# Optimization experiments

Hardware: AMD Instinct MI355X
Metric: run time of the kernel (lower is better)

Reference implementation:

```python
import jax, jax.numpy as jnp
import numpy as np

NUM_ITERATIONS = 3

def squash(t, axis=-1):
    sq = jnp.clip(jnp.sum(t * t, axis=axis, keepdims=True), 1e-8, 1e4)
    norm = jnp.sqrt(sq)
    scale = sq / (1.0 + sq)
    return scale * (t / (norm + 1e-8))

def setup_inputs() -> dict:
    key = jax.random.key(0)
    k1, k2 = jax.random.split(key)
    B, N_in, N_out, D_in, D_out = 128, 1152, 10, 8, 16
    u = jax.random.normal(k1, (B, N_in, D_in), dtype=jnp.float32)
    W = jax.random.normal(k2, (N_in, N_out, D_out, D_in), dtype=jnp.float32) * 0.005
    return {"u": u, "W": W}

def reference(u, W):
    # u: [B, N_in, D_in]; W: [N_in, N_out, D_out, D_in]
    # u_hat: [B, N_in, N_out, D_out]
    u_hat = jnp.einsum('iodk,bik->biod', W, u)
    u_hat = jnp.clip(u_hat, -10.0, 10.0)
    B, N_in, N_out, _ = u_hat.shape
    b = jnp.zeros((B, N_in, N_out), dtype=u_hat.dtype)
    v = None
    for it in range(NUM_ITERATIONS):
        c = jax.nn.softmax(b, axis=2)                      # [B, N_in, N_out]
        s = jnp.einsum('bio,biod->bod', c, u_hat)          # [B, N_out, D_out]
        v = squash(s, axis=-1)                             # [B, N_out, D_out]
        if it < NUM_ITERATIONS - 1:
            agreement = jnp.einsum('biod,bod->bio', u_hat, v)
            b = b + jnp.clip(agreement, -10.0, 10.0)
    return v
```

## Files before the change

kernel.cpp:

```cpp
#include <hip/hip_runtime.h>
#include <cstddef>

#define NB    128
#define NIN   1152
#define NOUT  10
#define DOUT  16
#define OD    160
#define NSEG  18
#define SEGI  64
#define PGRID (NB * NSEG)

typedef __attribute__((ext_vector_type(4))) unsigned int u32x4;

#if __has_builtin(__builtin_amdgcn_fdot2_f32_bf16)
#define HAS_DOT2 1
typedef __attribute__((ext_vector_type(2))) __bf16 bf16x2;
__device__ __forceinline__ float dot2bf(unsigned w, unsigned uu, float c) {
    return __builtin_amdgcn_fdot2_f32_bf16(
        __builtin_bit_cast(bf16x2, w), __builtin_bit_cast(bf16x2, uu), c, false);
}
#else
#define HAS_DOT2 0
#endif

__device__ __forceinline__ unsigned short f2bf(float x) {
    union { float f; unsigned u; } v; v.f = x;
    const unsigned r = v.u + 0x7fffu + ((v.u >> 16) & 1u);
    return (unsigned short)(r >> 16);
}
__device__ __forceinline__ unsigned pack2(float a, float b) {
    return (unsigned)f2bf(a) | ((unsigned)f2bf(b) << 16);
}
__device__ __forceinline__ float lo2f(unsigned w) {
    union { unsigned u; float f; } v; v.u = w << 16; return v.f;
}
__device__ __forceinline__ float hi2f(unsigned w) {
    union { unsigned u; float f; } v; v.u = w & 0xffff0000u; return v.f;
}

template<int CTRL>
__device__ __forceinline__ float dpp_f(float x) {
    return __int_as_float(__builtin_amdgcn_update_dpp(
        0, __float_as_int(x), CTRL, 0xF, 0xF, true));
}
__device__ __forceinline__ float row16_sum(float x) {
    x += dpp_f<0xB1>(x);
    x += dpp_f<0x4E>(x);
    x += dpp_f<0x124>(x);
    x += dpp_f<0x128>(x);
    return x;
}

__global__ __launch_bounds__(256)
void kprep(const float* __restrict__ W, unsigned* __restrict__ Wb)
{
    const int t = blockIdx.x * 256 + threadIdx.x;
    const float4 a = *reinterpret_cast<const float4*>(W + (size_t)t * 8);
    const float4 c = *reinterpret_cast<const float4*>(W + (size_t)t * 8 + 4);
    u32x4 o;
    o[0] = pack2(a.x, a.y); o[1] = pack2(a.z, a.w);
    o[2] = pack2(c.x, c.y); o[3] = pack2(c.z, c.w);
    *reinterpret_cast<u32x4*>(Wb + (size_t)t * 4) = o;
}

template<int PASS>
__global__ __launch_bounds__(256)
void kpass(const float* __restrict__ u, const unsigned* __restrict__ Wb,
           const float* __restrict__ p1, const float* __restrict__ p2,
           float* __restrict__ pout)
{
    __shared__ unsigned u_lds[SEGI * 4];
    __shared__ float red[16 * 176];
    __shared__ float sv1[OD], sv2[OD], vb[OD];

    const int tid = threadIdx.x;
    const int ip  = tid >> 4;
    const int dl  = tid & 15;
    const int seg = blockIdx.x >> 7;
    const int b   = blockIdx.x & 127;

    if (tid < 128) {
        const float4 a = *reinterpret_cast<const float4*>(
            u + ((size_t)b * NIN + seg * SEGI) * 8 + (size_t)tid * 4);
        u_lds[tid * 2]     = pack2(a.x, a.y);
        u_lds[tid * 2 + 1] = pack2(a.z, a.w);
    }

    if constexpr (PASS >= 2) {
        if (tid < OD) {
            float s = 0.0f;
            #pragma unroll
            for (int sg = 0; sg < NSEG; ++sg)
                s += p1[((size_t)b * NSEG + sg) * OD + tid];
            sv1[tid] = s;
            if constexpr (PASS == 3) {
                float s2 = 0.0f;
                #pragma unroll
                for (int sg = 0; sg < NSEG; ++sg)
                    s2 += p2[((size_t)b * NSEG + sg) * OD + tid];
                sv2[tid] = s2;
            }
        }
    }
    __syncthreads();
    if constexpr (PASS >= 2) {
        if (tid < OD) {
            const int o = tid >> 4;
            float ssq = 0.0f;
            #pragma unroll
            for (int dd = 0; dd < DOUT; ++dd) {
                const float x = sv1[o * DOUT + dd];
                ssq += x * x;
            }
            ssq = fminf(1e4f, fmaxf(1e-8f, ssq));
            float v = (ssq / (1.0f + ssq)) * sv1[tid] / (sqrtf(ssq) + 1e-8f);
            if constexpr (PASS == 3) {
                float sq2 = 0.0f;
                #pragma unroll
                for (int dd = 0; dd < DOUT; ++dd) {
                    const float x = sv2[o * DOUT + dd];
                    sq2 += x * x;
                }
                sq2 = fminf(1e4f, fmaxf(1e-8f, sq2));
                v += (sq2 / (1.0f + sq2)) * sv2[tid] / (sqrtf(sq2) + 1e-8f);
            }
            vb[tid] = v;
        }
    }
    __syncthreads();

    float vf[NOUT];
    if constexpr (PASS >= 2) {
        #pragma unroll
        for (int o = 0; o < NOUT; ++o) vf[o] = vb[o * DOUT + dl];
    }

    float acc[NOUT];
    #pragma unroll
    for (int o = 0; o < NOUT; ++o) acc[o] = 0.0f;

    for (int t = 0; t < 4; ++t) {
        const int i_loc = t * 16 + ip;
        const size_t i = (size_t)seg * SEGI + i_loc;

        const u32x4 uw = *reinterpret_cast<const u32x4*>(u_lds + i_loc * 4);
#if !HAS_DOT2
        float ur[8];
        #pragma unroll
        for (int kp = 0; kp < 4; ++kp) {
            ur[2 * kp]     = lo2f(uw[kp]);
            ur[2 * kp + 1] = hi2f(uw[kp]);
        }
#endif

        float uh[NOUT];
        #pragma unroll
        for (int o = 0; o < NOUT; ++o) {
            const u32x4 wv = *reinterpret_cast<const u32x4*>(
                Wb + ((i * NOUT + o) * DOUT + dl) * 4);
#if HAS_DOT2
            uh[o] = dot2bf(wv[0], uw[0],
                    dot2bf(wv[1], uw[1],
                    dot2bf(wv[2], uw[2],
                    dot2bf(wv[3], uw[3], 0.0f))));
#else
            uh[o] = lo2f(wv[0]) * ur[0] + hi2f(wv[0]) * ur[1]
                  + lo2f(wv[1]) * ur[2] + hi2f(wv[1]) * ur[3]
                  + lo2f(wv[2]) * ur[4] + hi2f(wv[2]) * ur[5]
                  + lo2f(wv[3]) * ur[6] + hi2f(wv[3]) * ur[7];
#endif
        }

        if constexpr (PASS == 1) {
            #pragma unroll
            for (int o = 0; o < NOUT; ++o) acc[o] += uh[o];
        } else {
            float cw[NOUT];
            float ssum = 0.0f;
            #pragma unroll
            for (int o = 0; o < NOUT; ++o) {
                const float e = __expf(row16_sum(uh[o] * vf[o]));
                cw[o] = e;
                ssum += e;
            }
            const float inv = 1.0f / ssum;
            #pragma unroll
            for (int o = 0; o < NOUT; ++o)
                acc[o] += (cw[o] * inv) * uh[o];
        }
    }

    #pragma unroll
    for (int o = 0; o < NOUT; ++o)
        red[ip * 176 + o * DOUT + dl] = acc[o];
    __syncthreads();
    if (tid < OD) {
        float r = 0.0f;
        #pragma unroll
        for (int k = 0; k < 16; ++k)
            r += red[k * 176 + tid];
        if constexpr (PASS == 1) r *= 0.1f;
        pout[((size_t)b * NSEG + seg) * OD + tid] = r;
    }
}

__global__ __launch_bounds__(256)
void kout(const float* __restrict__ p3, float* __restrict__ out)
{
    const int idx = blockIdx.x * 256 + threadIdx.x;
    const int b   = idx / OD;
    const int od  = idx - b * OD;
    float s = 0.0f;
    #pragma unroll
    for (int sg = 0; sg < NSEG; ++sg)
        s += p3[((size_t)b * NSEG + sg) * OD + od];

    const float sq0 = row16_sum(s * s);
    const float sq  = fminf(1e4f, fmaxf(1e-8f, sq0));
    out[idx] = (sq / (1.0f + sq)) * s / (sqrtf(sq) + 1e-8f);
}

extern "C" void kernel_launch(void* const* d_in, const int* in_sizes, int n_in,
                              void* d_out, int out_size, void* d_ws, size_t ws_size,
                              hipStream_t stream)
{
    const float* u = (const float*)d_in[0];
    const float* W = (const float*)d_in[1];
    float* out = (float*)d_out;

    unsigned* Wb = (unsigned*)d_ws;
    float* p1 = (float*)(Wb + (size_t)NIN * NOUT * DOUT * 4);
    float* p2 = p1 + (size_t)NB * NSEG * OD;
    float* p3 = p2 + (size_t)NB * NSEG * OD;

    kprep<<<720, 256, 0, stream>>>(W, Wb);
    kpass<1><<<PGRID, 256, 0, stream>>>(u, Wb, nullptr, nullptr, p1);
    kpass<2><<<PGRID, 256, 0, stream>>>(u, Wb, p1, nullptr, p2);
    kpass<3><<<PGRID, 256, 0, stream>>>(u, Wb, p1, p2, p3);
    kout<<<NB * OD / 256, 256, 0, stream>>>(p3, out);
}
```

Measured before the change: 65.06 us.

## Process two batch items per block to reuse each W load

Each block now handles a pair of batch elements over a smaller 32-input segment, so every bf16 W vector loaded from global memory feeds two dot products. Grid size stays the same (64 pairs x 36 segments), and the per-batch partial count doubles to 36 segments. This halves W traffic per unit of work but doubles the register footprint for accumulators and uh values, and increases the partial-sum reduction reads in later passes.

```diff
diff --git a/kernel.cpp b/kernel.cpp
--- a/kernel.cpp
+++ b/kernel.cpp
@@ -6,9 +6,9 @@
 #define NOUT  10
 #define DOUT  16
 #define OD    160
-#define NSEG  18
-#define SEGI  64
-#define PGRID (NB * NSEG)
+#define NSEG  36
+#define SEGI  32
+#define PGRID (NB / 2 * NSEG)
 
 typedef __attribute__((ext_vector_type(4))) unsigned int u32x4;
 
@@ -69,138 +69,165 @@
            const float* __restrict__ p1, const float* __restrict__ p2,
            float* __restrict__ pout)
 {
-    __shared__ unsigned u_lds[SEGI * 4];
-    __shared__ float red[16 * 176];
-    __shared__ float sv1[OD], sv2[OD], vb[OD];
-
-    const int tid = threadIdx.x;
-    const int ip  = tid >> 4;
-    const int dl  = tid & 15;
-    const int seg = blockIdx.x >> 7;
-    const int b   = blockIdx.x & 127;
+    __shared__ unsigned u_lds[2][SEGI * 4];
+    __shared__ float red[2][16][176];
+    __shared__ float sv1[2][OD], sv2[2][OD], vb[2][OD];
+
+    const int tid   = threadIdx.x;
+    const int ip    = tid >> 4;
+    const int dl    = tid & 15;
+    const int seg   = blockIdx.x >> 6;
+    const int bpair = blockIdx.x & 63;
+    const int b0    = bpair * 2;
 
     if (tid < 128) {
+        const int bb = tid >> 6;
+        const int t2 = tid & 63;
         const float4 a = *reinterpret_cast<const float4*>(
-            u + ((size_t)b * NIN + seg * SEGI) * 8 + (size_t)tid * 4);
-        u_lds[tid * 2]     = pack2(a.x, a.y);
-        u_lds[tid * 2 + 1] = pack2(a.z, a.w);
+            u + ((size_t)(b0 + bb) * NIN + seg * SEGI) * 8 + (size_t)t2 * 4);
+        u_lds[bb][t2 * 2]     = pack2(a.x, a.y);
+        u_lds[bb][t2 * 2 + 1] = pack2(a.z, a.w);
     }
 
     if constexpr (PASS >= 2) {
-        if (tid < OD) {
+        for (int t = tid; t < 2 * OD; t += 256) {
+            const int bb = t / OD;
+            const int od = t - bb * OD;
             float s = 0.0f;
             #pragma unroll
             for (int sg = 0; sg < NSEG; ++sg)
-                s += p1[((size_t)b * NSEG + sg) * OD + tid];
-            sv1[tid] = s;
+                s += p1[((size_t)(b0 + bb) * NSEG + sg) * OD + od];
+            sv1[bb][od] = s;
             if constexpr (PASS == 3) {
                 float s2 = 0.0f;
                 #pragma unroll
                 for (int sg = 0; sg < NSEG; ++sg)
-                    s2 += p2[((size_t)b * NSEG + sg) * OD + tid];
-                sv2[tid] = s2;
+                    s2 += p2[((size_t)(b0 + bb) * NSEG + sg) * OD + od];
+                sv2[bb][od] = s2;
             }
         }
     }
     __syncthreads();
     if constexpr (PASS >= 2) {
-        if (tid < OD) {
-            const int o = tid >> 4;
+        for (int t = tid; t < 2 * OD; t += 256) {
+            const int bb = t / OD;
+            const int od = t - bb * OD;
+            const int o  = od >> 4;
             float ssq = 0.0f;
             #pragma unroll
             for (int dd = 0; dd < DOUT; ++dd) {
-                const float x = sv1[o * DOUT + dd];
+                const float x = sv1[bb][o * DOUT + dd];
                 ssq += x * x;
             }
             ssq = fminf(1e4f, fmaxf(1e-8f, ssq));
-            float v = (ssq / (1.0f + ssq)) * sv1[tid] / (sqrtf(ssq) + 1e-8f);
+            float v = (ssq / (1.0f + ssq)) * sv1[bb][od] / (sqrtf(ssq) + 1e-8f);
             if constexpr (PASS == 3) {
                 float sq2 = 0.0f;
                 #pragma unroll
                 for (int dd = 0; dd < DOUT; ++dd) {
-                    const float x = sv2[o * DOUT + dd];
+                    const float x = sv2[bb][o * DOUT + dd];
                     sq2 += x * x;
                 }
                 sq2 = fminf(1e4f, fmaxf(1e-8f, sq2));
-                v += (sq2 / (1.0f + sq2)) * sv2[tid] / (sqrtf(sq2) + 1e-8f);
-            }
-            vb[tid] = v;
-        }
-    }
-    __syncthreads();
-
-    float vf[NOUT];
+                v += (sq2 / (1.0f + sq2)) * sv2[bb][od] / (sqrtf(sq2) + 1e-8f);
+            }
+            vb[bb][od] = v;
+        }
+        __syncthreads();
+    }
+
+    float vf0[NOUT], vf1[NOUT];
     if constexpr (PASS >= 2) {
         #pragma unroll
-        for (int o = 0; o < NOUT; ++o) vf[o] = vb[o * DOUT + dl];
-    }
-
-    float acc[NOUT];
+        for (int o = 0; o < NOUT; ++o) {
+            vf0[o] = vb[0][o * DOUT + dl];
+            vf1[o] = vb[1][o * DOUT + dl];
+        }
+    }
+    if constexpr (PASS == 1) __syncthreads();
+
+    float acc0[NOUT], acc1[NOUT];
     #pragma unroll
-    for (int o = 0; o < NOUT; ++o) acc[o] = 0.0f;
-
-    for (int t = 0; t < 4; ++t) {
+    for (int o = 0; o < NOUT; ++o) { acc0[o] = 0.0f; acc1[o] = 0.0f; }
+
+    for (int t = 0; t < 2; ++t) {
         const int i_loc = t * 16 + ip;
         const size_t i = (size_t)seg * SEGI + i_loc;
 
-        const u32x4 uw = *reinterpret_cast<const u32x4*>(u_lds + i_loc * 4);
+        const u32x4 uw0 = *reinterpret_cast<const u32x4*>(&u_lds[0][i_loc * 4]);
+        const u32x4 uw1 = *reinterpret_cast<const u32x4*>(&u_lds[1][i_loc * 4]);
 #if !HAS_DOT2
-        float ur[8];
+        float ur0[8], ur1[8];
         #pragma unroll
         for (int kp = 0; kp < 4; ++kp) {
-            ur[2 * kp]     = lo2f(uw[kp]);
-            ur[2 * kp + 1] = hi2f(uw[kp]);
+            ur0[2 * kp] = lo2f(uw0[kp]); ur0[2 * kp + 1] = hi2f(uw0[kp]);
+            ur1[2 * kp] = lo2f(uw1[kp]); ur1[2 * kp + 1] = hi2f(uw1[kp]);
         }
 #endif
 
-        float uh[NOUT];
+        float uh0[NOUT], uh1[NOUT];
         #pragma unroll
         for (int o = 0; o < NOUT; ++o) {
             const u32x4 wv = *reinterpret_cast<const u32x4*>(
                 Wb + ((i * NOUT + o) * DOUT + dl) * 4);
 #if HAS_DOT2
-            uh[o] = dot2bf(wv[0], uw[0],
-                    dot2bf(wv[1], uw[1],
-                    dot2bf(wv[2], uw[2],
-                    dot2bf(wv[3], uw[3], 0.0f))));
+            uh0[o] = dot2bf(wv[0], uw0[0], dot2bf(wv[1], uw0[1],
+                     dot2bf(wv[2], uw0[2], dot2bf(wv[3], uw0[3], 0.0f))));
+            uh1[o] = dot2bf(wv[0], uw1[0], dot2bf(wv[1], uw1[1],
+                     dot2bf(wv[2], uw1[2], dot2bf(wv[3], uw1[3], 0.0f))));
 #else
-            uh[o] = lo2f(wv[0]) * ur[0] + hi2f(wv[0]) * ur[1]
-                  + lo2f(wv[1]) * ur[2] + hi2f(wv[1]) * ur[3]
-                  + lo2f(wv[2]) * ur[4] + hi2f(wv[2]) * ur[5]
-                  + lo2f(wv[3]) * ur[6] + hi2f(wv[3]) * ur[7];
+            uh0[o] = lo2f(wv[0]) * ur0[0] + hi2f(wv[0]) * ur0[1]
+                   + lo2f(wv[1]) * ur0[2] + hi2f(wv[1]) * ur0[3]
+                   + lo2f(wv[2]) * ur0[4] + hi2f(wv[2]) * ur0[5]
+                   + lo2f(wv[3]) * ur0[6] + hi2f(wv[3]) * ur0[7];
+            uh1[o] = lo2f(wv[0]) * ur1[0] + hi2f(wv[0]) * ur1[1]
+                   + lo2f(wv[1]) * ur1[2] + hi2f(wv[1]) * ur1[3]
+                   + lo2f(wv[2]) * ur1[4] + hi2f(wv[2]) * ur1[5]
+                   + lo2f(wv[3]) * ur1[6] + hi2f(wv[3]) * ur1[7];
 #endif
         }
 
         if constexpr (PASS == 1) {
             #pragma unroll
-            for (int o = 0; o < NOUT; ++o) acc[o] += uh[o];
+            for (int o = 0; o < NOUT; ++o) {
+                acc0[o] += uh0[o];
+                acc1[o] += uh1[o];
+            }
         } else {
-            float cw[NOUT];
-            float ssum = 0.0f;
+            float cw0[NOUT], cw1[NOUT];
+            float ssum0 = 0.0f, ssum1 = 0.0f;
             #pragma unroll
             for (int o = 0; o < NOUT; ++o) {
-                const float e = __expf(row16_sum(uh[o] * vf[o]));
-                cw[o] = e;
-                ssum += e;
-            }
-            const float inv = 1.0f / ssum;
-            #pragma unroll
-            for (int o = 0; o < NOUT; ++o)
-                acc[o] += (cw[o] * inv) * uh[o];
+                const float e0 = __expf(row16_sum(uh0[o] * vf0[o]));
+                const float e1 = __expf(row16_sum(uh1[o] * vf1[o]));
+                cw0[o] = e0; ssum0 += e0;
+                cw1[o] = e1; ssum1 += e1;
+            }
+            const float inv0 = 1.0f / ssum0;
+            const float inv1 = 1.0f / ssum1;
+            #pragma unroll
+            for (int o = 0; o < NOUT; ++o) {
+                acc0[o] += (cw0[o] * inv0) * uh0[o];
+                acc1[o] += (cw1[o] * inv1) * uh1[o];
+            }
         }
     }
 
     #pragma unroll
-    for (int o = 0; o < NOUT; ++o)
-        red[ip * 176 + o * DOUT + dl] = acc[o];
+    for (int o = 0; o < NOUT; ++o) {
+        red[0][ip][o * DOUT + dl] = acc0[o];
+        red[1][ip][o * DOUT + dl] = acc1[o];
+    }
     __syncthreads();
-    if (tid < OD) {
+    for (int t = tid; t < 2 * OD; t += 256) {
+        const int bb = t / OD;
+        const int od = t - bb * OD;
         float r = 0.0f;
         #pragma unroll
         for (int k = 0; k < 16; ++k)
-            r += red[k * 176 + tid];
+            r += red[bb][k][od];
         if constexpr (PASS == 1) r *= 0.1f;
-        pout[((size_t)b * NSEG + seg) * OD + tid] = r;
+        pout[((size_t)(b0 + bb) * NSEG + seg) * OD + od] = r;
     }
 }
 
```

Result: no change. 65.39 us (+0.5%).
